# Kernel optimization log

Measured on AMD Instinct MI355X. Metric: run time of the kernel, lower is better.

## Reference

```python
import jax, jax.numpy as jnp
import numpy as np

B, C, H, W = 8, 512, 32, 32
NH, DH = 8, 64          # num_heads, head_dim (C = NH*DH)
GROUPS, EPS = 32, 1e-5


def group_norm(x, gamma, beta):
    b, c, h, w = x.shape
    xg = x.reshape(b, GROUPS, c // GROUPS, h, w)
    mu = xg.mean(axis=(2, 3, 4), keepdims=True)
    var = xg.var(axis=(2, 3, 4), keepdims=True)
    xn = ((xg - mu) * jax.lax.rsqrt(var + EPS)).reshape(b, c, h, w)
    return xn * gamma[:, None, None] + beta[:, None, None]


def conv1x1(x, w, b):
    # x: [B,C,H,W], w: [O,C], b: [O]
    return jnp.einsum('bchw,oc->bohw', x, w) + b[:, None, None]


def setup_inputs() -> dict:
    key = jax.random.key(0)
    ks = jax.random.split(key, 5)
    return {
        'x': jax.random.normal(ks[0], (B, C, H, W), jnp.float32),
        'norm_gamma': jnp.ones((C,), jnp.float32),
        'norm_beta': jnp.zeros((C,), jnp.float32),
        'qkv_w': jax.random.normal(ks[1], (3 * C, C), jnp.float32) * (1.0 / np.sqrt(C)),
        'qkv_b': jax.random.normal(ks[2], (3 * C,), jnp.float32) * 0.02,
        'proj_w': jax.random.normal(ks[3], (C, C), jnp.float32) * (1.0 / np.sqrt(C)),
        'proj_b': jax.random.normal(ks[4], (C,), jnp.float32) * 0.02,
    }


def reference(x, norm_gamma, norm_beta, qkv_w, qkv_b, proj_w, proj_b):
    scale = DH ** -0.5
    h = group_norm(x, norm_gamma, norm_beta)
    qkv = conv1x1(h, qkv_w, qkv_b)                       # [B,3C,H,W]
    qkv = qkv.reshape(B, 3, NH, DH, H * W)
    qkv = jnp.transpose(qkv, (1, 0, 2, 4, 3))            # [3,B,NH,HW,DH]
    q, k, v = qkv[0], qkv[1], qkv[2]
    attn = jnp.einsum('bhid,bhjd->bhij', q, k) * scale   # [B,NH,HW,HW]
    attn = jax.nn.softmax(attn, axis=-1)
    h = jnp.einsum('bhij,bhjd->bhid', attn, v)           # [B,NH,HW,DH]
    # faithful to torch: direct row-major reshape [B,NH,HW,DH] -> [B,C,H,W]
    h = h.reshape(B, C, H, W)
    h = conv1x1(h, proj_w, proj_b)
    return x + h
```

## Files before the change

kernel.cpp:

```cpp
#include <hip/hip_runtime.h>


typedef float  f32x4  __attribute__((ext_vector_type(4)));
typedef float  f32x16 __attribute__((ext_vector_type(16)));
typedef __bf16 bf16x8 __attribute__((ext_vector_type(8)));
typedef __bf16 bf16x4 __attribute__((ext_vector_type(4)));
typedef __bf16 bf16x2 __attribute__((ext_vector_type(2)));
typedef unsigned u32x4 __attribute__((ext_vector_type(4)));

#define MFMA(a, b, c)   __builtin_amdgcn_mfma_f32_16x16x32_bf16(a, b, c, 0, 0, 0)
#define MFMA32(a, b, c) __builtin_amdgcn_mfma_f32_32x32x16_bf16(a, b, c, 0, 0, 0)

__device__ __forceinline__ void async16(const __bf16* g, __bf16* l) {
  __builtin_amdgcn_global_load_lds((const __attribute__((address_space(1))) void*)g,
                                   (__attribute__((address_space(3))) void*)l, 16, 0, 0);
}

__device__ __forceinline__ int chk(int n, int c) {
  return ((((n >> 6) * 16 + (c >> 5)) * 4 + ((c >> 3) & 3)) * 512) + (n & 63) * 8 + (c & 7);
}

__device__ __forceinline__ unsigned pk2(float x, float y) {
  bf16x2 t; t[0] = (__bf16)x; t[1] = (__bf16)y;
  return __builtin_bit_cast(unsigned, t);
}

__global__ __launch_bounds__(512) void prep_k(const float* __restrict__ x,
                                              const float* __restrict__ gamma,
                                              const float* __restrict__ beta,
                                              __bf16* __restrict__ Hout,
                                              const float* __restrict__ qw, __bf16* __restrict__ dq,
                                              const float* __restrict__ pw, __bf16* __restrict__ dp) {
  __shared__ __bf16 xs[16 * 1032];
  __shared__ float  red[16];
  __shared__ float  ga[16], be[16], stat[2];
  const int tid = threadIdx.x;

  if (blockIdx.x >= 256) {
    int i = ((blockIdx.x - 256) * 512 + tid) * 4;
    const float* src = (i < 786432) ? qw : pw;
    __bf16* dst = (i < 786432) ? dq : dp;
    int j = (i < 786432) ? i : (i - 786432);
    int m = j >> 9, k = j & 511;
    float4 v = *(const float4*)(src + j);
    bf16x4 o;
    o[0] = (__bf16)v.x; o[1] = (__bf16)v.y; o[2] = (__bf16)v.z; o[3] = (__bf16)v.w;
    *(bf16x4*)(dst + chk(m, k)) = o;
    return;
  }

  const int w = tid >> 6, l = tid & 63;
  const int bg = blockIdx.x, b = bg >> 5, g = bg & 31, c0 = g * 16;
  const float* xg = x + b * 524288 + c0 * 1024;

  float sum = 0.f, sq = 0.f;
#pragma unroll
  for (int p = 0; p < 8; p++) {
    int idx = p * 2048 + tid * 4;
    float4 v = *(const float4*)(xg + idx);
    int c = idx >> 10, s = idx & 1023;
    bf16x4 o;
    o[0] = (__bf16)v.x; o[1] = (__bf16)v.y; o[2] = (__bf16)v.z; o[3] = (__bf16)v.w;
    *(bf16x4*)(&xs[c * 1032 + s]) = o;
    sum += v.x + v.y + v.z + v.w;
    sq  += v.x * v.x + v.y * v.y + v.z * v.z + v.w * v.w;
  }
#pragma unroll
  for (int o = 32; o > 0; o >>= 1) { sum += __shfl_down(sum, o); sq += __shfl_down(sq, o); }
  if (l == 0) { red[w * 2] = sum; red[w * 2 + 1] = sq; }
  __syncthreads();
  if (tid == 0) {
    float S = 0.f, Q = 0.f;
#pragma unroll
    for (int i = 0; i < 8; i++) { S += red[i * 2]; Q += red[i * 2 + 1]; }
    float mean = S * (1.f / 16384.f);
    float var  = Q * (1.f / 16384.f) - mean * mean;
    stat[0] = mean; stat[1] = rsqrtf(var + 1e-5f);
  }
  if (tid < 16) { ga[tid] = gamma[c0 + tid]; be[tid] = beta[c0 + tid]; }
  __syncthreads();
  const float mean = stat[0], rstd = stat[1];
#pragma unroll
  for (int p = 0; p < 2; p++) {
    int s = p * 512 + tid;
    int n = b * 1024 + s;
    bf16x8 o0, o1;
#pragma unroll
    for (int c = 0; c < 8; c++) {
      float f = (float)xs[c * 1032 + s];
      o0[c] = (__bf16)((f - mean) * rstd * ga[c] + be[c]);
    }
#pragma unroll
    for (int c = 8; c < 16; c++) {
      float f = (float)xs[c * 1032 + s];
      o1[c - 8] = (__bf16)((f - mean) * rstd * ga[c] + be[c]);
    }
    *(bf16x8*)(Hout + chk(n, c0)) = o0;
    *(bf16x8*)(Hout + chk(n, c0 + 8)) = o1;
  }
}

__global__ __launch_bounds__(256) void gemm_qkv_k(const __bf16* __restrict__ W,
                                                  const float* __restrict__ bias,
                                                  const __bf16* __restrict__ H,
                                                  __bf16* __restrict__ qbuf,
                                                  __bf16* __restrict__ kbuf,
                                                  __bf16* __restrict__ vt) {
  __shared__ union {
    struct { __bf16 a[2][4096]; __bf16 b[2][4096]; } ab;
    __bf16 cs[128 * 136];
  } lds;
  const int tid = threadIdx.x;
  const int w = tid >> 6, l = tid & 63, quad = l >> 4, li = l & 15;
  const int wr = w >> 1, wc = w & 1;
  const int mblk = blockIdx.x >> 6, nblk = blockIdx.x & 63;
  const int m0 = mblk * 128, n0 = nblk * 128;

  f32x4 acc[4][4];
#pragma unroll
  for (int i = 0; i < 4; i++)
#pragma unroll
    for (int j = 0; j < 4; j++) acc[i][j] = f32x4{0.f, 0.f, 0.f, 0.f};

  const __bf16* Ag = W + (((m0 >> 6) * 16) * 4 + w) * 512 + l * 8;
  const __bf16* Bg = H + (((n0 >> 6) * 16) * 4 + w) * 512 + l * 8;
  const int halfA = 16 * 4 * 512;

  async16(Ag,         &lds.ab.a[0][w * 1024]);
  async16(Ag + halfA, &lds.ab.a[0][w * 1024 + 512]);
  async16(Bg,         &lds.ab.b[0][w * 1024]);
  async16(Bg + halfA, &lds.ab.b[0][w * 1024 + 512]);

#pragma unroll 1
  for (int kt = 0; kt < 16; kt++) {
    int cur = kt & 1, nxt = cur ^ 1;
    __syncthreads();
    if (kt < 15) {
      int ko = (kt + 1) * 2048;
      async16(Ag + ko,          &lds.ab.a[nxt][w * 1024]);
      async16(Ag + halfA + ko,  &lds.ab.a[nxt][w * 1024 + 512]);
      async16(Bg + ko,          &lds.ab.b[nxt][w * 1024]);
      async16(Bg + halfA + ko,  &lds.ab.b[nxt][w * 1024 + 512]);
    }
    bf16x8 af[4], bfr[4];
#pragma unroll
    for (int i = 0; i < 4; i++)
      af[i] = *(const bf16x8*)(&lds.ab.a[cur][quad * 1024 + (wr * 64 + i * 16 + li) * 8]);
#pragma unroll
    for (int i = 0; i < 4; i++)
      bfr[i] = *(const bf16x8*)(&lds.ab.b[cur][quad * 1024 + (wc * 64 + i * 16 + li) * 8]);
#pragma unroll
    for (int i = 0; i < 4; i++)
#pragma unroll
      for (int j = 0; j < 4; j++) acc[i][j] = MFMA(af[i], bfr[j], acc[i][j]);
  }

  const int t = m0 >> 9;
  const int cbase = m0 & 511;
  __syncthreads();
#pragma unroll
  for (int mi = 0; mi < 4; mi++) {
    int olocal = wr * 64 + mi * 16 + quad * 4;
    float bs[4];
#pragma unroll
    for (int r = 0; r < 4; r++) bs[r] = bias[m0 + olocal + r];
#pragma unroll
    for (int ni = 0; ni < 4; ni++) {
      int nlocal = wc * 64 + ni * 16 + li;
      bf16x4 pk;
#pragma unroll
      for (int r = 0; r < 4; r++) {
        float f = acc[mi][ni][r] + bs[r];
        if (t == 0) f *= 0.180336880f;
        pk[r] = (__bf16)f;
      }
      *(bf16x4*)(&lds.cs[nlocal * 136 + olocal]) = pk;
    }
  }
  __syncthreads();
  const int bb = n0 >> 10, s0 = n0 & 1023;
  if (t < 2) {
    __bf16* dst = (t == 0) ? qbuf : kbuf;
    const int nh0 = cbase >> 6;
#pragma unroll
    for (int p = 0; p < 8; p++) {
      int idx = p * 256 + tid;
      int oc = idx & 15, nloc = idx >> 4;
      uint4 val = *(const uint4*)(&lds.cs[nloc * 136 + oc * 8]);
      int bh = bb * 8 + nh0 + (oc >> 3);
      int s = s0 + nloc, d0 = (oc & 7) * 8;
      *(uint4*)(dst + (((bh * 16 + (s >> 6)) * 8 + (d0 >> 3)) * 64 + (s & 63)) * 8) = val;
    }
  } else {
#pragma unroll
    for (int p = 0; p < 8; p++) {
      int idx = p * 256 + tid;
      int o = idx & 127, ng = idx >> 7;
      int c = cbase + o, nh2 = c >> 6, d = c & 63;
      int bh = bb * 8 + nh2;
      int j0 = s0 + ng * 8;
      bf16x8 vv;
#pragma unroll
      for (int jj = 0; jj < 8; jj++) vv[jj] = lds.cs[(ng * 8 + jj) * 136 + o];
      *(bf16x8*)(vt + (((bh * 16 + (j0 >> 6)) * 8 + ((j0 >> 3) & 7)) * 64 + d) * 8) = vv;
    }
  }
}

__global__ __launch_bounds__(256) void attn_k(const __bf16* __restrict__ qb,
                                              const __bf16* __restrict__ kb,
                                              const __bf16* __restrict__ vt,
                                              __bf16* __restrict__ pin) {
  __shared__ __bf16 KC[2][4096];
  __shared__ __bf16 VC[2][4096];
  const int tid = threadIdx.x;
  const int w = tid >> 6, l = tid & 63, hi = l >> 5, i32 = l & 31;
  const int x = blockIdx.x;
  const int qt = (x >> 3) & 7;
  const int bh = (x & 7) | ((x >> 6) << 3);
  const int b = bh >> 3, nh = bh & 7;
  const __bf16* Qg = qb + bh * 65536;
  const __bf16* Kg = kb + bh * 65536;
  const __bf16* Vg = vt + bh * 65536;

#pragma unroll
  for (int p = 0; p < 2; p++) {
    int ch = w + 4 * p;
    async16(Kg + ch * 512 + l * 8, &KC[0][ch * 512 + l * 8]);
    async16(Vg + ch * 512 + l * 8, &VC[0][ch * 512 + l * 8]);
  }
  const int s = qt * 128 + w * 32 + i32;
  bf16x8 qf[4];
#pragma unroll
  for (int ks = 0; ks < 4; ks++)
    qf[ks] = *(const bf16x8*)(Qg + ((s >> 6) * 8 + ks * 2 + hi) * 512 + (s & 63) * 8);
  __syncthreads();

  float lsum = 0.f;
  f32x16 oacc[2];
#pragma unroll
  for (int r = 0; r < 16; r++) { oacc[0][r] = 0.f; oacc[1][r] = 0.f; }

#pragma unroll 1
  for (int kv = 0; kv < 16; kv++) {
    int cur = kv & 1, nxt = cur ^ 1;
    if (kv < 15) {
#pragma unroll
      for (int p = 0; p < 2; p++) {
        int ch = w + 4 * p;
        async16(Kg + (kv + 1) * 4096 + ch * 512 + l * 8, &KC[nxt][ch * 512 + l * 8]);
        async16(Vg + (kv + 1) * 4096 + ch * 512 + l * 8, &VC[nxt][ch * 512 + l * 8]);
      }
    }

#pragma unroll
    for (int jt = 0; jt < 2; jt++) {
      f32x16 st;
#pragma unroll
      for (int r = 0; r < 16; r++) st[r] = 0.f;
#pragma unroll
      for (int ks = 0; ks < 4; ks++) {
        bf16x8 kf = *(const bf16x8*)(&KC[cur][(ks * 2 + hi) * 512 + (jt * 32 + i32) * 8]);
        st = MFMA32(kf, qf[ks], st);
      }
      float pr[16];
#pragma unroll
      for (int r = 0; r < 16; r++) pr[r] = __builtin_amdgcn_exp2f(st[r]);
#pragma unroll
      for (int r = 0; r < 16; r += 4) lsum += (pr[r] + pr[r + 1]) + (pr[r + 2] + pr[r + 3]);
#pragma unroll
      for (int h = 0; h < 2; h++) {
        unsigned u0 = pk2(pr[8 * h + 0], pr[8 * h + 1]);
        unsigned u1 = pk2(pr[8 * h + 2], pr[8 * h + 3]);
        unsigned v0 = pk2(pr[8 * h + 4], pr[8 * h + 5]);
        unsigned v1 = pk2(pr[8 * h + 6], pr[8 * h + 7]);
        asm volatile("v_permlane32_swap_b32 %0, %1" : "+v"(u0), "+v"(v0));
        asm volatile("v_permlane32_swap_b32 %0, %1" : "+v"(u1), "+v"(v1));
        u32x4 dv; dv[0] = u0; dv[1] = u1; dv[2] = v0; dv[3] = v1;
        bf16x8 pf = __builtin_bit_cast(bf16x8, dv);
        int js = jt * 2 + h;
#pragma unroll
        for (int dt = 0; dt < 2; dt++) {
          bf16x8 vf = *(const bf16x8*)(&VC[cur][(js * 2 + hi) * 512 + (dt * 32 + i32) * 8]);
          oacc[dt] = MFMA32(pf, vf, oacc[dt]);
        }
      }
    }
    __syncthreads();
  }

  lsum += __shfl_xor(lsum, 32);
  const float inv = 1.f / lsum;

  char* PO = (char*)KC;
#pragma unroll
  for (int dt = 0; dt < 2; dt++) {
#pragma unroll
    for (int r = 0; r < 8; r++) {
      int ilo = (r & 3) + 8 * (r >> 2) + 4 * hi;
      float iblo = __shfl(inv, ilo);
      float ibhi = __shfl(inv, ilo + 16);
      bf16x2 ov;
      ov[0] = (__bf16)(oacc[dt][r]     * iblo);
      ov[1] = (__bf16)(oacc[dt][r + 8] * ibhi);
      *(bf16x2*)(PO + (ilo * 64 + dt * 32 + i32) * 16 + w * 4) = ov;
    }
  }
  __syncthreads();
  __bf16* Pg = pin + (nh * 8 + qt) * 65536 + b * 8192;
#pragma unroll
  for (int p = 0; p < 4; p++) {
    int idx = p * 256 + tid;
    *(bf16x8*)(Pg + idx * 8) = *(const bf16x8*)((const char*)PO + idx * 16);
  }
}

__global__ __launch_bounds__(256) void gemm_proj_k(const __bf16* __restrict__ W,
                                                   const float* __restrict__ bias,
                                                   const __bf16* __restrict__ P,
                                                   const float* __restrict__ x,
                                                   float* __restrict__ out) {
  __shared__ __bf16 AL[2][2048];
  __shared__ __bf16 BL[2][4096];
  const int tid = threadIdx.x;
  const int w = tid >> 6, l = tid & 63, quad = l >> 4, li = l & 15;
  const int wr = w >> 1, wc = w & 1;
  const int mblk = blockIdx.x >> 6, nblk = blockIdx.x & 63;
  const int m0 = mblk * 64, n0 = nblk * 128;

  f32x4 acc[2][4];
#pragma unroll
  for (int i = 0; i < 2; i++)
#pragma unroll
    for (int j = 0; j < 4; j++) acc[i][j] = f32x4{0.f, 0.f, 0.f, 0.f};

  const __bf16* Ag = W + ((mblk * 16) * 4 + w) * 512 + l * 8;
  const __bf16* Bg = P + w * 65536 + (n0 + l) * 8;

  async16(Ag,       &AL[0][w * 512]);
  async16(Bg,       &BL[0][w * 1024]);
  async16(Bg + 512, &BL[0][w * 1024 + 512]);

#pragma unroll 1
  for (int kt = 0; kt < 16; kt++) {
    int cur = kt & 1, nxt = cur ^ 1;
    __syncthreads();
    if (kt < 15) {
      int koA = (kt + 1) * 2048;
      int koB = (kt + 1) * 262144;
      async16(Ag + koA,       &AL[nxt][w * 512]);
      async16(Bg + koB,       &BL[nxt][w * 1024]);
      async16(Bg + koB + 512, &BL[nxt][w * 1024 + 512]);
    }
    bf16x8 af[2], bfr[4];
#pragma unroll
    for (int i = 0; i < 2; i++)
      af[i] = *(const bf16x8*)(&AL[cur][quad * 512 + (wr * 32 + i * 16 + li) * 8]);
#pragma unroll
    for (int j = 0; j < 4; j++)
      bfr[j] = *(const bf16x8*)(&BL[cur][quad * 1024 + (wc * 64 + j * 16 + li) * 8]);
#pragma unroll
    for (int i = 0; i < 2; i++)
#pragma unroll
      for (int j = 0; j < 4; j++) acc[i][j] = MFMA(af[i], bfr[j], acc[i][j]);
  }

  const int bb = n0 >> 10;
#pragma unroll
  for (int mi = 0; mi < 2; mi++) {
    int o = m0 + wr * 32 + mi * 16 + quad * 4;
    float bs[4];
#pragma unroll
    for (int r = 0; r < 4; r++) bs[r] = bias[o + r];
#pragma unroll
    for (int ni = 0; ni < 4; ni++) {
      int n = n0 + wc * 64 + ni * 16 + li;
      int s = n & 1023;
#pragma unroll
      for (int r = 0; r < 4; r++) {
        int a = (bb * 512 + o + r) * 1024 + s;
        out[a] = acc[mi][ni][r] + bs[r] + x[a];
      }
    }
  }
}

extern "C" void kernel_launch(void* const* d_in, const int* in_sizes, int n_in,
                              void* d_out, int out_size, void* d_ws, size_t ws_size,
                              hipStream_t stream) {
  const float* x      = (const float*)d_in[0];
  const float* gamma  = (const float*)d_in[1];
  const float* beta   = (const float*)d_in[2];
  const float* qkv_w  = (const float*)d_in[3];
  const float* qkv_b  = (const float*)d_in[4];
  const float* proj_w = (const float*)d_in[5];
  const float* proj_b = (const float*)d_in[6];

  __bf16* ws   = (__bf16*)d_ws;
  __bf16* H    = ws;
  __bf16* qbuf = ws + 4194304;
  __bf16* kbuf = ws + 8388608;
  __bf16* vt   = ws + 12582912;
  __bf16* wq   = ws + 16777216;
  __bf16* wp   = ws + 17563648;

  prep_k<<<768, 512, 0, stream>>>(x, gamma, beta, H, qkv_w, wq, proj_w, wp);
  gemm_qkv_k<<<768, 256, 0, stream>>>(wq, qkv_b, H, qbuf, kbuf, vt);
  attn_k<<<512, 256, 0, stream>>>(qbuf, kbuf, vt, H);
  gemm_proj_k<<<512, 256, 0, stream>>>(wp, proj_b, H, x, (float*)d_out);
}
```

Baseline: 139.7 us.

## Split attention KV tiles across two wave halves with 512-thread blocks

The attention kernel now runs 8 waves per block. Each pair of waves shares a 32-row query slice and splits each 64-key tile into halves, so per-wave work per iteration halves and more waves can hide latency. Partial row sums and output accumulators are combined through shared memory at the end. This adds extra barriers and an fp32 reduction pass through LDS, and the launch bound may force register pressure.

```diff
diff --git a/kernel.cpp b/kernel.cpp
--- a/kernel.cpp
+++ b/kernel.cpp
@@ -207,14 +207,17 @@
   }
 }
 
-__global__ __launch_bounds__(256) void attn_k(const __bf16* __restrict__ qb,
-                                              const __bf16* __restrict__ kb,
-                                              const __bf16* __restrict__ vt,
-                                              __bf16* __restrict__ pin) {
-  __shared__ __bf16 KC[2][4096];
-  __shared__ __bf16 VC[2][4096];
+__global__ __launch_bounds__(512, 4) void attn_k(const __bf16* __restrict__ qb,
+                                                 const __bf16* __restrict__ kb,
+                                                 const __bf16* __restrict__ vt,
+                                                 __bf16* __restrict__ pin) {
+  __shared__ __align__(16) char smem[33792];
+  __bf16 (*KC)[4096] = (__bf16(*)[4096])smem;
+  __bf16 (*VC)[4096] = (__bf16(*)[4096])(smem + 16384);
+  float* lred        = (float*)(smem + 32768);
   const int tid = threadIdx.x;
   const int w = tid >> 6, l = tid & 63, hi = l >> 5, i32 = l & 31;
+  const int g = w >> 1, jh = w & 1;
   const int x = blockIdx.x;
   const int qt = (x >> 3) & 7;
   const int bh = (x & 7) | ((x >> 6) << 3);
@@ -223,13 +226,10 @@
   const __bf16* Kg = kb + bh * 65536;
   const __bf16* Vg = vt + bh * 65536;
 
-#pragma unroll
-  for (int p = 0; p < 2; p++) {
-    int ch = w + 4 * p;
-    async16(Kg + ch * 512 + l * 8, &KC[0][ch * 512 + l * 8]);
-    async16(Vg + ch * 512 + l * 8, &VC[0][ch * 512 + l * 8]);
-  }
-  const int s = qt * 128 + w * 32 + i32;
+  async16(Kg + w * 512 + l * 8, &KC[0][w * 512 + l * 8]);
+  async16(Vg + w * 512 + l * 8, &VC[0][w * 512 + l * 8]);
+
+  const int s = qt * 128 + g * 32 + i32;
   bf16x8 qf[4];
 #pragma unroll
   for (int ks = 0; ks < 4; ks++)
@@ -245,72 +245,89 @@
   for (int kv = 0; kv < 16; kv++) {
     int cur = kv & 1, nxt = cur ^ 1;
     if (kv < 15) {
-#pragma unroll
-      for (int p = 0; p < 2; p++) {
-        int ch = w + 4 * p;
-        async16(Kg + (kv + 1) * 4096 + ch * 512 + l * 8, &KC[nxt][ch * 512 + l * 8]);
-        async16(Vg + (kv + 1) * 4096 + ch * 512 + l * 8, &VC[nxt][ch * 512 + l * 8]);
-      }
-    }
-
-#pragma unroll
-    for (int jt = 0; jt < 2; jt++) {
-      f32x16 st;
-#pragma unroll
-      for (int r = 0; r < 16; r++) st[r] = 0.f;
-#pragma unroll
-      for (int ks = 0; ks < 4; ks++) {
-        bf16x8 kf = *(const bf16x8*)(&KC[cur][(ks * 2 + hi) * 512 + (jt * 32 + i32) * 8]);
-        st = MFMA32(kf, qf[ks], st);
-      }
-      float pr[16];
-#pragma unroll
-      for (int r = 0; r < 16; r++) pr[r] = __builtin_amdgcn_exp2f(st[r]);
-#pragma unroll
-      for (int r = 0; r < 16; r += 4) lsum += (pr[r] + pr[r + 1]) + (pr[r + 2] + pr[r + 3]);
-#pragma unroll
-      for (int h = 0; h < 2; h++) {
-        unsigned u0 = pk2(pr[8 * h + 0], pr[8 * h + 1]);
-        unsigned u1 = pk2(pr[8 * h + 2], pr[8 * h + 3]);
-        unsigned v0 = pk2(pr[8 * h + 4], pr[8 * h + 5]);
-        unsigned v1 = pk2(pr[8 * h + 6], pr[8 * h + 7]);
-        asm volatile("v_permlane32_swap_b32 %0, %1" : "+v"(u0), "+v"(v0));
-        asm volatile("v_permlane32_swap_b32 %0, %1" : "+v"(u1), "+v"(v1));
-        u32x4 dv; dv[0] = u0; dv[1] = u1; dv[2] = v0; dv[3] = v1;
-        bf16x8 pf = __builtin_bit_cast(bf16x8, dv);
-        int js = jt * 2 + h;
-#pragma unroll
-        for (int dt = 0; dt < 2; dt++) {
-          bf16x8 vf = *(const bf16x8*)(&VC[cur][(js * 2 + hi) * 512 + (dt * 32 + i32) * 8]);
-          oacc[dt] = MFMA32(pf, vf, oacc[dt]);
-        }
+      async16(Kg + (kv + 1) * 4096 + w * 512 + l * 8, &KC[nxt][w * 512 + l * 8]);
+      async16(Vg + (kv + 1) * 4096 + w * 512 + l * 8, &VC[nxt][w * 512 + l * 8]);
+    }
+
+    f32x16 st;
+#pragma unroll
+    for (int r = 0; r < 16; r++) st[r] = 0.f;
+#pragma unroll
+    for (int ks = 0; ks < 4; ks++) {
+      bf16x8 kf = *(const bf16x8*)(&KC[cur][(ks * 2 + hi) * 512 + (jh * 32 + i32) * 8]);
+      st = MFMA32(kf, qf[ks], st);
+    }
+    float pr[16];
+#pragma unroll
+    for (int r = 0; r < 16; r++) pr[r] = __builtin_amdgcn_exp2f(st[r]);
+#pragma unroll
+    for (int r = 0; r < 16; r += 4) lsum += (pr[r] + pr[r + 1]) + (pr[r + 2] + pr[r + 3]);
+#pragma unroll
+    for (int h = 0; h < 2; h++) {
+      unsigned u0 = pk2(pr[8 * h + 0], pr[8 * h + 1]);
+      unsigned u1 = pk2(pr[8 * h + 2], pr[8 * h + 3]);
+      unsigned v0 = pk2(pr[8 * h + 4], pr[8 * h + 5]);
+      unsigned v1 = pk2(pr[8 * h + 6], pr[8 * h + 7]);
+      asm volatile("v_permlane32_swap_b32 %0, %1" : "+v"(u0), "+v"(v0));
+      asm volatile("v_permlane32_swap_b32 %0, %1" : "+v"(u1), "+v"(v1));
+      u32x4 dv; dv[0] = u0; dv[1] = u1; dv[2] = v0; dv[3] = v1;
+      bf16x8 pf = __builtin_bit_cast(bf16x8, dv);
+      int js = jh * 2 + h;
+#pragma unroll
+      for (int dt = 0; dt < 2; dt++) {
+        bf16x8 vf = *(const bf16x8*)(&VC[cur][(js * 2 + hi) * 512 + (dt * 32 + i32) * 8]);
+        oacc[dt] = MFMA32(pf, vf, oacc[dt]);
       }
     }
     __syncthreads();
   }
 
   lsum += __shfl_xor(lsum, 32);
-  const float inv = 1.f / lsum;
-
-  char* PO = (char*)KC;
-#pragma unroll
-  for (int dt = 0; dt < 2; dt++) {
-#pragma unroll
-    for (int r = 0; r < 8; r++) {
-      int ilo = (r & 3) + 8 * (r >> 2) + 4 * hi;
-      float iblo = __shfl(inv, ilo);
-      float ibhi = __shfl(inv, ilo + 16);
-      bf16x2 ov;
-      ov[0] = (__bf16)(oacc[dt][r]     * iblo);
-      ov[1] = (__bf16)(oacc[dt][r + 8] * ibhi);
-      *(bf16x2*)(PO + (ilo * 64 + dt * 32 + i32) * 16 + w * 4) = ov;
-    }
+  if (l < 32) lred[w * 32 + i32] = lsum;
+  __syncthreads();
+  const float inv = 1.f / (lred[w * 32 + i32] + lred[(w ^ 1) * 32 + i32]);
+
+  float* OB = (float*)smem;
+  if (jh == 1) {
+#pragma unroll
+    for (int dt = 0; dt < 2; dt++)
+#pragma unroll
+      for (int r = 0; r < 8; r++) {
+        int ilo = (r & 3) + 8 * (r >> 2) + 4 * hi;
+        OB[(g * 32 + ilo) * 64 + dt * 32 + i32]      = oacc[dt][r];
+        OB[(g * 32 + ilo + 16) * 64 + dt * 32 + i32] = oacc[dt][r + 8];
+      }
+  }
+  __syncthreads();
+  bf16x2 ov[2][8];
+  if (jh == 0) {
+#pragma unroll
+    for (int dt = 0; dt < 2; dt++)
+#pragma unroll
+      for (int r = 0; r < 8; r++) {
+        int ilo = (r & 3) + 8 * (r >> 2) + 4 * hi;
+        float iblo = __shfl(inv, ilo);
+        float ibhi = __shfl(inv, ilo + 16);
+        ov[dt][r][0] = (__bf16)((oacc[dt][r]     + OB[(g * 32 + ilo) * 64 + dt * 32 + i32])      * iblo);
+        ov[dt][r][1] = (__bf16)((oacc[dt][r + 8] + OB[(g * 32 + ilo + 16) * 64 + dt * 32 + i32]) * ibhi);
+      }
+  }
+  __syncthreads();
+  char* PO = smem;
+  if (jh == 0) {
+#pragma unroll
+    for (int dt = 0; dt < 2; dt++)
+#pragma unroll
+      for (int r = 0; r < 8; r++) {
+        int ilo = (r & 3) + 8 * (r >> 2) + 4 * hi;
+        *(bf16x2*)(PO + (ilo * 64 + dt * 32 + i32) * 16 + g * 4) = ov[dt][r];
+      }
   }
   __syncthreads();
   __bf16* Pg = pin + (nh * 8 + qt) * 65536 + b * 8192;
 #pragma unroll
-  for (int p = 0; p < 4; p++) {
-    int idx = p * 256 + tid;
+  for (int p = 0; p < 2; p++) {
+    int idx = p * 512 + tid;
     *(bf16x8*)(Pg + idx * 8) = *(const bf16x8*)((const char*)PO + idx * 16);
   }
 }
@@ -406,6 +423,6 @@
 
   prep_k<<<768, 512, 0, stream>>>(x, gamma, beta, H, qkv_w, wq, proj_w, wp);
   gemm_qkv_k<<<768, 256, 0, stream>>>(wq, qkv_b, H, qbuf, kbuf, vt);
-  attn_k<<<512, 256, 0, stream>>>(qbuf, kbuf, vt, H);
+  attn_k<<<512, 512, 0, stream>>>(qbuf, kbuf, vt, H);
   gemm_proj_k<<<512, 256, 0, stream>>>(wp, proj_b, H, x, (float*)d_out);
 }
```

Result: no change. 137.5 us (-1.6%).
